# Kernel tuning notes

Measured on AMD Instinct MI355X. Metric: run time of the kernel, lower is better.

## Reference

```python
import jax, jax.numpy as jnp
import numpy as np

B, N, DIN, DOUT = 16384, 32, 128, 256
ITERS = 3
SQUASH_W = 1.0
EPS_SQUASH = 1e-9
EPS_NORM = 1e-12


def setup_inputs() -> dict:
    key = jax.random.key(0)
    k1, k2, k3 = jax.random.split(key, 3)
    embeds = jax.random.normal(k1, (B, N, DIN), dtype=jnp.float32)
    weights = jax.random.normal(k2, (B, N), dtype=jnp.float32)
    # xavier_normal init for Linear weight, zero-ish bias (torch default bias is
    # uniform but value is irrelevant for a correctness baseline; keep it small)
    xav = float(np.sqrt(2.0 / (DIN + DOUT)))
    W = jax.random.normal(k3, (DIN, DOUT), dtype=jnp.float32) * xav
    b = jnp.zeros((DOUT,), dtype=jnp.float32)
    return {"embeds": embeds, "weights": weights, "W": W, "b": b}


def _squash(s):
    # s: [B, D]; squash along the capsule vector dim D (axis=-2 in the original
    # [B,1,1,D,1] layout == last axis here).
    sq = jnp.sum(s * s, axis=-1, keepdims=True)
    scale = sq / (SQUASH_W + sq) / jnp.sqrt(sq + EPS_SQUASH)
    return scale * s


def reference(embeds, weights, W, b):
    # Linear + (eval-mode) dropout identity; no activation (default None)
    x = jnp.einsum("bni,io->bno", embeds, W) + b          # [B, N, DOUT]
    # F.normalize(p=2, dim=-2) over the capsule vector dim
    nrm = jnp.sqrt(jnp.sum(x * x, axis=-1, keepdims=True))
    u_hat = x / jnp.maximum(nrm, EPS_NORM)                 # [B, N, DOUT]
    u_hat_det = jax.lax.stop_gradient(u_hat)

    b_ij = weights[:, :, None]                             # [B, N, 1]
    c_ij = None
    v = None
    for r in range(ITERS):
        c_ij = jax.nn.softmax(b_ij, axis=1) * N            # [B, N, 1]
        s = jnp.sum(c_ij * u_hat, axis=1)                  # [B, DOUT]
        v = _squash(s)                                     # [B, DOUT]
        if r < ITERS - 1:
            # u_hat^T v  -> per-candidate agreement scalar
            agree = jnp.einsum("bnd,bd->bn", u_hat_det, v)
            b_ij = b_ij + agree[:, :, None]
    poses = v                                              # [B, DOUT]
    c_out = c_ij[:, :, 0]                                  # [B, N]
    return (poses, c_out)
```

## Files before the change

### kernel.cpp

```cpp
#include <hip/hip_runtime.h>

typedef _Float16 f16;
typedef __attribute__((ext_vector_type(8))) _Float16 f16x8;
typedef __attribute__((ext_vector_type(4))) _Float16 f16x4;
typedef __attribute__((ext_vector_type(4))) float  f32x4;

#define B_    16384
#define N_    32
#define DIN_  128
#define DOUT_ 256

__device__ __forceinline__ float rdlane(float v, int lane) {
    return __uint_as_float(__builtin_amdgcn_readlane(__float_as_uint(v), lane));
}
__device__ __forceinline__ float red32(float v) {
    v += __shfl_xor(v, 1); v += __shfl_xor(v, 2); v += __shfl_xor(v, 4);
    v += __shfl_xor(v, 8); v += __shfl_xor(v, 16);
    return v;
}
__device__ __forceinline__ int xidx(int n, int o) {
    return n * 272 + (o ^ ((n & 7) << 3));
}

__global__ void prep_w(const float* __restrict__ W, f16* __restrict__ wp) {
    int tid = blockIdx.x * 256 + threadIdx.x;
    int ks = tid >> 10;
    int ot = (tid >> 6) & 15;
    int l  = tid & 63;
    int k0 = ks * 32 + ((l >> 4) << 3);
    int o  = ot * 16 + (l & 15);
    f16 v[8];
#pragma unroll
    for (int j = 0; j < 8; ++j) v[j] = (f16)W[(size_t)(k0 + j) * DOUT_ + o];
    *reinterpret_cast<f16x8*>(&wp[(size_t)tid * 8]) = *reinterpret_cast<f16x8*>(v);
}

#define PLANE_ 17408

__global__ __launch_bounds__(256, 4) void dyr_main(
    const float* __restrict__ embeds, const float* __restrict__ weights,
    const f16* __restrict__ wp,       const float* __restrict__ bias,
    float* __restrict__ out)
{
    __shared__ __align__(16) char pool[39584];
    f16*   elds = reinterpret_cast<f16*>(pool);
    f16*   xh   = reinterpret_cast<f16*>(pool);
    f16*   xe   = reinterpret_cast<f16*>(pool + PLANE_);
    float* glds = reinterpret_cast<float*>(pool + 2 * PLANE_);
    float* cpls = reinterpret_cast<float*>(pool + 2 * PLANE_ + 4624);
    float* scls = cpls + 32;

    const int tid = threadIdx.x;
    const int w   = tid >> 6;
    const int l   = tid & 63;
    const int col = l & 15;
    const int q   = l >> 4;
    const int b   = blockIdx.x;
    const int n0  = l & 31;

    float bval = (w == 0) ? weights[(size_t)b * N_ + n0] : 0.f;

    const float4* e4 = reinterpret_cast<const float4*>(embeds + (size_t)b * N_ * DIN_);
#pragma unroll
    for (int p = 0; p < 4; ++p) {
        int fi = p * 256 + tid;
        float4 v = e4[fi];
        int m = fi >> 5;
        int k = (fi & 31) << 2;
        f16 pk[4] = { (f16)v.x, (f16)v.y, (f16)v.z, (f16)v.w };
        *reinterpret_cast<f16x4*>(&elds[m * 136 + k]) = *reinterpret_cast<f16x4*>(pk);
    }
    __syncthreads();

    f32x4 acc[2][4];
#pragma unroll
    for (int mt = 0; mt < 2; ++mt)
#pragma unroll
        for (int t = 0; t < 4; ++t) acc[mt][t] = (f32x4){0.f, 0.f, 0.f, 0.f};

    const int aoff0 = col * 136 + (q << 3);
#pragma unroll
    for (int ks = 0; ks < 4; ++ks) {
        f16x8 a0 = *reinterpret_cast<const f16x8*>(&elds[aoff0 + ks * 32]);
        f16x8 a1 = *reinterpret_cast<const f16x8*>(&elds[aoff0 + 16 * 136 + ks * 32]);
#pragma unroll
        for (int t = 0; t < 4; ++t) {
            f16x8 bf = *reinterpret_cast<const f16x8*>(
                &wp[((size_t)((ks * 16) + (w * 4 + t)) * 64 + l) * 8]);
            acc[0][t] = __builtin_amdgcn_mfma_f32_16x16x32_f16(a0, bf, acc[0][t], 0, 0, 0);
            acc[1][t] = __builtin_amdgcn_mfma_f32_16x16x32_f16(a1, bf, acc[1][t], 0, 0, 0);
        }
    }
#pragma unroll
    for (int t = 0; t < 4; ++t) {
        float bv = bias[w * 64 + t * 16 + col];
#pragma unroll
        for (int mt = 0; mt < 2; ++mt)
#pragma unroll
            for (int r = 0; r < 4; ++r) acc[mt][t][r] += bv;
    }
    __syncthreads();

#pragma unroll
    for (int mt = 0; mt < 2; ++mt)
#pragma unroll
        for (int t = 0; t < 4; ++t) {
            int o = w * 64 + t * 16 + col;
#pragma unroll
            for (int r = 0; r < 4; ++r) {
                float xv = acc[mt][t][r];
                f16 h = (f16)xv;
                f16 e = (f16)(xv - (float)h);
                int idx = xidx(mt * 16 + q * 4 + r, o);
                xh[idx] = h;
                xe[idx] = e;
            }
        }
    __syncthreads();

    {
        const int mi = w >> 1, ni = w & 1;
        f32x4 gacc = (f32x4){0.f, 0.f, 0.f, 0.f};
#pragma unroll
        for (int ks = 0; ks < 8; ++ks) {
            int ra = xidx(mi * 16 + col, ks * 32 + (q << 3));
            f16x8 ha = *reinterpret_cast<const f16x8*>(&xh[ra]);
            f16x8 ea = *reinterpret_cast<const f16x8*>(&xe[ra]);
            f16x8 hb = ha, eb = ea;
            if (mi != ni) {
                int rb = xidx(ni * 16 + col, ks * 32 + (q << 3));
                hb = *reinterpret_cast<const f16x8*>(&xh[rb]);
                eb = *reinterpret_cast<const f16x8*>(&xe[rb]);
            }
            gacc = __builtin_amdgcn_mfma_f32_16x16x32_f16(ha, hb, gacc, 0, 0, 0);
            gacc = __builtin_amdgcn_mfma_f32_16x16x32_f16(ha, eb, gacc, 0, 0, 0);
            gacc = __builtin_amdgcn_mfma_f32_16x16x32_f16(ea, hb, gacc, 0, 0, 0);
        }
#pragma unroll
        for (int r = 0; r < 4; ++r)
            glds[(mi * 16 + q * 4 + r) * 36 + ni * 16 + col] = gacc[r];
    }
    __syncthreads();

    float cval = 0.f, scale = 0.f, rn = 0.f;
    if (w == 0) {
        float dv = glds[n0 * 36 + n0];
        rn = rsqrtf(fmaxf(dv, 1e-24f));

        float g[32];
#pragma unroll
        for (int j8 = 0; j8 < 8; ++j8) {
            f32x4 gv = *reinterpret_cast<const f32x4*>(&glds[n0 * 36 + j8 * 4]);
#pragma unroll
            for (int r = 0; r < 4; ++r) g[j8 * 4 + r] = gv[r] * rn;
        }
#pragma unroll
        for (int j = 0; j < 32; ++j) g[j] *= rdlane(rn, j);

        for (int it = 0; it < 3; ++it) {
            float mx = bval;
            mx = fmaxf(mx, __shfl_xor(mx, 1));  mx = fmaxf(mx, __shfl_xor(mx, 2));
            mx = fmaxf(mx, __shfl_xor(mx, 4));  mx = fmaxf(mx, __shfl_xor(mx, 8));
            mx = fmaxf(mx, __shfl_xor(mx, 16));
            float ex = __expf(bval - mx);
            float sm = red32(ex);
            cval = ex * (32.0f / sm);
            float t0 = 0.f, t1 = 0.f;
#pragma unroll
            for (int j = 0; j < 32; j += 2) {
                t0 = fmaf(g[j],     rdlane(cval, j),     t0);
                t1 = fmaf(g[j + 1], rdlane(cval, j + 1), t1);
            }
            float t = t0 + t1;
            float sq = red32(cval * t);
            scale = sq / ((1.0f + sq) * sqrtf(sq + 1e-9f));
            if (it < 2) bval = fmaf(scale, t, bval);
        }

        if (l < 32) {
            cpls[l] = cval * rn;
            out[(size_t)B_ * DOUT_ + (size_t)b * N_ + l] = cval;
        }
        if (l == 0) *scls = scale;
    }
    __syncthreads();

    {
        float sc = *scls;
        float cv[2][4];
#pragma unroll
        for (int mt = 0; mt < 2; ++mt)
#pragma unroll
            for (int r = 0; r < 4; ++r) cv[mt][r] = cpls[mt * 16 + q * 4 + r];
#pragma unroll
        for (int t = 0; t < 4; ++t) {
            float s = 0.f;
#pragma unroll
            for (int mt = 0; mt < 2; ++mt)
#pragma unroll
                for (int r = 0; r < 4; ++r) s = fmaf(cv[mt][r], acc[mt][t][r], s);
            s += __shfl_xor(s, 16);
            s += __shfl_xor(s, 32);
            if (l < 16) out[(size_t)b * DOUT_ + w * 64 + t * 16 + l] = sc * s;
        }
    }
}

extern "C" void kernel_launch(void* const* d_in, const int* in_sizes, int n_in,
                              void* d_out, int out_size, void* d_ws, size_t ws_size,
                              hipStream_t stream) {
    const float* embeds  = (const float*)d_in[0];
    const float* weights = (const float*)d_in[1];
    const float* W       = (const float*)d_in[2];
    const float* bias    = (const float*)d_in[3];
    float* out = (float*)d_out;
    f16* wp = (f16*)d_ws;

    prep_w<<<16, 256, 0, stream>>>(W, wp);
    dyr_main<<<B_, 256, 0, stream>>>(embeds, weights, wp, bias, out);
}
```

Measured before the change: 432.3 us.

## Transpose GEMM tiles, halve x LDS staging in two chunks, raise occupancy

The first GEMM now computes x transposed (W fragments as the A operand), so each lane holds 4 consecutive output columns. This allows packed f16x4 LDS stores and a vectorized bias load. The hi/lo split of x is staged in LDS in two 128-column halves, with the Gram accumulation done chunk by chunk. That cuts the shared pool from about 39.6KB to 22KB and lets launch bounds go from 4 to 6 blocks per CU. The final weighted sum uses a butterfly transpose-reduce across lanes instead of cross-quad shuffles per tile. The cost is extra barriers and more shuffle/select work in the epilogue.

```diff
diff --git a/kernel.cpp b/kernel.cpp
--- a/kernel.cpp
+++ b/kernel.cpp
@@ -18,8 +18,8 @@
     v += __shfl_xor(v, 8); v += __shfl_xor(v, 16);
     return v;
 }
-__device__ __forceinline__ int xidx(int n, int o) {
-    return n * 272 + (o ^ ((n & 7) << 3));
+__device__ __forceinline__ int xidx(int n, int oc) {
+    return n * 136 + (oc ^ ((n & 7) << 3));
 }
 
 __global__ void prep_w(const float* __restrict__ W, f16* __restrict__ wp) {
@@ -35,19 +35,22 @@
     *reinterpret_cast<f16x8*>(&wp[(size_t)tid * 8]) = *reinterpret_cast<f16x8*>(v);
 }
 
-#define PLANE_ 17408
-
-__global__ __launch_bounds__(256, 4) void dyr_main(
+#define XH_OFF_   0
+#define XE_OFF_   8704
+#define GLDS_OFF_ 17408
+#define CPLS_OFF_ 22032
+
+__global__ __launch_bounds__(256, 6) void dyr_main(
     const float* __restrict__ embeds, const float* __restrict__ weights,
     const f16* __restrict__ wp,       const float* __restrict__ bias,
     float* __restrict__ out)
 {
-    __shared__ __align__(16) char pool[39584];
+    __shared__ __align__(16) char pool[22176];
     f16*   elds = reinterpret_cast<f16*>(pool);
-    f16*   xh   = reinterpret_cast<f16*>(pool);
-    f16*   xe   = reinterpret_cast<f16*>(pool + PLANE_);
-    float* glds = reinterpret_cast<float*>(pool + 2 * PLANE_);
-    float* cpls = reinterpret_cast<float*>(pool + 2 * PLANE_ + 4624);
+    f16*   xh   = reinterpret_cast<f16*>(pool + XH_OFF_);
+    f16*   xe   = reinterpret_cast<f16*>(pool + XE_OFF_);
+    float* glds = reinterpret_cast<float*>(pool + GLDS_OFF_);
+    float* cpls = reinterpret_cast<float*>(pool + CPLS_OFF_);
     float* scls = cpls + 32;
 
     const int tid = threadIdx.x;
@@ -72,57 +75,61 @@
     }
     __syncthreads();
 
-    f32x4 acc[2][4];
-#pragma unroll
-    for (int mt = 0; mt < 2; ++mt)
-#pragma unroll
-        for (int t = 0; t < 4; ++t) acc[mt][t] = (f32x4){0.f, 0.f, 0.f, 0.f};
-
-    const int aoff0 = col * 136 + (q << 3);
+    f32x4 acc[4][2];
+#pragma unroll
+    for (int ot = 0; ot < 4; ++ot)
+#pragma unroll
+        for (int nt = 0; nt < 2; ++nt) acc[ot][nt] = (f32x4){0.f, 0.f, 0.f, 0.f};
+
+    const int boff0 = col * 136 + (q << 3);
 #pragma unroll
     for (int ks = 0; ks < 4; ++ks) {
-        f16x8 a0 = *reinterpret_cast<const f16x8*>(&elds[aoff0 + ks * 32]);
-        f16x8 a1 = *reinterpret_cast<const f16x8*>(&elds[aoff0 + 16 * 136 + ks * 32]);
-#pragma unroll
-        for (int t = 0; t < 4; ++t) {
-            f16x8 bf = *reinterpret_cast<const f16x8*>(
-                &wp[((size_t)((ks * 16) + (w * 4 + t)) * 64 + l) * 8]);
-            acc[0][t] = __builtin_amdgcn_mfma_f32_16x16x32_f16(a0, bf, acc[0][t], 0, 0, 0);
-            acc[1][t] = __builtin_amdgcn_mfma_f32_16x16x32_f16(a1, bf, acc[1][t], 0, 0, 0);
-        }
-    }
-#pragma unroll
-    for (int t = 0; t < 4; ++t) {
-        float bv = bias[w * 64 + t * 16 + col];
-#pragma unroll
-        for (int mt = 0; mt < 2; ++mt)
-#pragma unroll
-            for (int r = 0; r < 4; ++r) acc[mt][t][r] += bv;
-    }
-    __syncthreads();
-
-#pragma unroll
-    for (int mt = 0; mt < 2; ++mt)
-#pragma unroll
-        for (int t = 0; t < 4; ++t) {
-            int o = w * 64 + t * 16 + col;
-#pragma unroll
-            for (int r = 0; r < 4; ++r) {
-                float xv = acc[mt][t][r];
-                f16 h = (f16)xv;
-                f16 e = (f16)(xv - (float)h);
-                int idx = xidx(mt * 16 + q * 4 + r, o);
-                xh[idx] = h;
-                xe[idx] = e;
-            }
-        }
-    __syncthreads();
-
-    {
-        const int mi = w >> 1, ni = w & 1;
-        f32x4 gacc = (f32x4){0.f, 0.f, 0.f, 0.f};
-#pragma unroll
-        for (int ks = 0; ks < 8; ++ks) {
+        f16x8 b0 = *reinterpret_cast<const f16x8*>(&elds[boff0 + ks * 32]);
+        f16x8 b1 = *reinterpret_cast<const f16x8*>(&elds[boff0 + 16 * 136 + ks * 32]);
+#pragma unroll
+        for (int ot = 0; ot < 4; ++ot) {
+            f16x8 wf = *reinterpret_cast<const f16x8*>(
+                &wp[((size_t)((ks * 16) + (w * 4 + ot)) * 64 + l) * 8]);
+            acc[ot][0] = __builtin_amdgcn_mfma_f32_16x16x32_f16(wf, b0, acc[ot][0], 0, 0, 0);
+            acc[ot][1] = __builtin_amdgcn_mfma_f32_16x16x32_f16(wf, b1, acc[ot][1], 0, 0, 0);
+        }
+    }
+#pragma unroll
+    for (int ot = 0; ot < 4; ++ot) {
+        f32x4 bb = *reinterpret_cast<const f32x4*>(&bias[w * 64 + ot * 16 + (q << 2)]);
+#pragma unroll
+        for (int nt = 0; nt < 2; ++nt)
+#pragma unroll
+            for (int r = 0; r < 4; ++r) acc[ot][nt][r] += bb[r];
+    }
+    __syncthreads();
+
+    const int mi = w >> 1, ni = w & 1;
+    f32x4 gacc = (f32x4){0.f, 0.f, 0.f, 0.f};
+#pragma unroll
+    for (int c = 0; c < 2; ++c) {
+        if ((w >> 1) == c) {
+#pragma unroll
+            for (int ot = 0; ot < 4; ++ot)
+#pragma unroll
+                for (int nt = 0; nt < 2; ++nt) {
+                    int n  = nt * 16 + col;
+                    int oc = (w & 1) * 64 + ot * 16 + (q << 2);
+                    f16 hv[4], ev[4];
+#pragma unroll
+                    for (int r = 0; r < 4; ++r) {
+                        float xv = acc[ot][nt][r];
+                        hv[r] = (f16)xv;
+                        ev[r] = (f16)(xv - (float)hv[r]);
+                    }
+                    int idx = xidx(n, oc);
+                    *reinterpret_cast<f16x4*>(&xh[idx]) = *reinterpret_cast<f16x4*>(hv);
+                    *reinterpret_cast<f16x4*>(&xe[idx]) = *reinterpret_cast<f16x4*>(ev);
+                }
+        }
+        __syncthreads();
+#pragma unroll
+        for (int ks = 0; ks < 4; ++ks) {
             int ra = xidx(mi * 16 + col, ks * 32 + (q << 3));
             f16x8 ha = *reinterpret_cast<const f16x8*>(&xh[ra]);
             f16x8 ea = *reinterpret_cast<const f16x8*>(&xe[ra]);
@@ -136,10 +143,11 @@
             gacc = __builtin_amdgcn_mfma_f32_16x16x32_f16(ha, eb, gacc, 0, 0, 0);
             gacc = __builtin_amdgcn_mfma_f32_16x16x32_f16(ea, hb, gacc, 0, 0, 0);
         }
-#pragma unroll
-        for (int r = 0; r < 4; ++r)
-            glds[(mi * 16 + q * 4 + r) * 36 + ni * 16 + col] = gacc[r];
-    }
+        if (c == 0) __syncthreads();
+    }
+#pragma unroll
+    for (int r = 0; r < 4; ++r)
+        glds[(mi * 16 + q * 4 + r) * 36 + ni * 16 + col] = gacc[r];
     __syncthreads();
 
     float cval = 0.f, scale = 0.f, rn = 0.f;
@@ -187,22 +195,57 @@
 
     {
         float sc = *scls;
-        float cv[2][4];
-#pragma unroll
-        for (int mt = 0; mt < 2; ++mt)
-#pragma unroll
-            for (int r = 0; r < 4; ++r) cv[mt][r] = cpls[mt * 16 + q * 4 + r];
-#pragma unroll
-        for (int t = 0; t < 4; ++t) {
-            float s = 0.f;
-#pragma unroll
-            for (int mt = 0; mt < 2; ++mt)
-#pragma unroll
-                for (int r = 0; r < 4; ++r) s = fmaf(cv[mt][r], acc[mt][t][r], s);
-            s += __shfl_xor(s, 16);
-            s += __shfl_xor(s, 32);
-            if (l < 16) out[(size_t)b * DOUT_ + w * 64 + t * 16 + l] = sc * s;
-        }
+        float c0 = cpls[col];
+        float c1 = cpls[16 + col];
+        float cur[16];
+#pragma unroll
+        for (int ot = 0; ot < 4; ++ot)
+#pragma unroll
+            for (int r = 0; r < 4; ++r)
+                cur[ot * 4 + r] = fmaf(c0, acc[ot][0][r], c1 * acc[ot][1][r]);
+
+        float k8[8], s8[8];
+        {
+            const bool hi = (col & 8) != 0;
+#pragma unroll
+            for (int i = 0; i < 8; ++i) {
+                k8[i] = hi ? cur[i + 8] : cur[i];
+                s8[i] = hi ? cur[i] : cur[i + 8];
+            }
+#pragma unroll
+            for (int i = 0; i < 8; ++i) k8[i] += __shfl_xor(s8[i], 8);
+        }
+        float k4[4], s4[4];
+        {
+            const bool hi = (col & 4) != 0;
+#pragma unroll
+            for (int i = 0; i < 4; ++i) {
+                k4[i] = hi ? k8[i + 4] : k8[i];
+                s4[i] = hi ? k8[i] : k8[i + 4];
+            }
+#pragma unroll
+            for (int i = 0; i < 4; ++i) k4[i] += __shfl_xor(s4[i], 4);
+        }
+        float k2[2], s2[2];
+        {
+            const bool hi = (col & 2) != 0;
+#pragma unroll
+            for (int i = 0; i < 2; ++i) {
+                k2[i] = hi ? k4[i + 2] : k4[i];
+                s2[i] = hi ? k4[i] : k4[i + 2];
+            }
+#pragma unroll
+            for (int i = 0; i < 2; ++i) k2[i] += __shfl_xor(s2[i], 2);
+        }
+        float k1, s1;
+        {
+            const bool hi = (col & 1) != 0;
+            k1 = hi ? k2[1] : k2[0];
+            s1 = hi ? k2[0] : k2[1];
+            k1 += __shfl_xor(s1, 1);
+        }
+        int o = (col >> 2) * 16 + (q << 2) + (col & 3);
+        out[(size_t)b * DOUT_ + w * 64 + o] = sc * k1;
     }
 }
 
```

Result: slower. 625.0 us (+44.6%).
